# Kernel optimization log

Hardware: AMD Instinct MI355X
Metric: run time of the kernel (lower is better)

Reference implementation:

```python
import jax, jax.numpy as jnp
import numpy as np

B, N, C, NT = 32, 512, 32, 24   # batch, frames, channels-per-token, tokens
H, DH = 8, 48                   # heads, dim_head (DH % NT == 0 -> CS = 2)
E = H * DH                      # encode_dim = 384
IN = C * NT                     # in_dim = 768
OUT = 768                       # out_dim


def setup_inputs() -> dict:
    key = jax.random.key(0)
    ks = jax.random.split(key, 12)
    s = lambda fan_in: 1.0 / np.sqrt(fan_in)
    return {
        "x": jax.random.normal(ks[0], (B, N, C, NT), dtype=jnp.float32),
        "Wqkv_t": jax.random.uniform(ks[1], (IN, 3 * E), jnp.float32, -s(IN), s(IN)),
        "bqkv_t": jax.random.uniform(ks[2], (3 * E,), jnp.float32, -s(IN), s(IN)),
        "Wqkv_s": jax.random.uniform(ks[3], (IN, 3 * E), jnp.float32, -s(IN), s(IN)),
        "bqkv_s": jax.random.uniform(ks[4], (3 * E,), jnp.float32, -s(IN), s(IN)),
        "Wts": jax.random.uniform(ks[5], (2 * E, 2 * E), jnp.float32, -s(2 * E), s(2 * E)),
        "bts": jax.random.uniform(ks[6], (2 * E,), jnp.float32, -s(2 * E), s(2 * E)),
        "Wfc_t": jax.random.uniform(ks[7], (E, OUT), jnp.float32, -s(E), s(E)),
        "bfc_t": jax.random.uniform(ks[8], (OUT,), jnp.float32, -s(E), s(E)),
        "Wfc_s": jax.random.uniform(ks[9], (E, OUT), jnp.float32, -s(E), s(E)),
        "bfc_s": jax.random.uniform(ks[10], (OUT,), jnp.float32, -s(E), s(E)),
    }


def reference(x, Wqkv_t, bqkv_t, Wqkv_s, bqkv_s, Wts, bts, Wfc_t, bfc_t, Wfc_s, bfc_s):
    b, n, c, nt = x.shape
    cs = DH // nt  # channels per token inside a head (=2)
    xf = x.reshape(b, n, c * nt)                       # (b, n, in_dim)

    # --- temporal attention over the n (frame) axis ---
    qkv_t = (xf @ Wqkv_t + bqkv_t).reshape(b, n, 3, H, DH)
    qkv_t = jnp.transpose(qkv_t, (2, 0, 3, 1, 4))      # (3, b, H, n, DH)
    qt, kt, vt = qkv_t[0], qkv_t[1], qkv_t[2]
    attn_t = jax.nn.softmax(
        jnp.einsum('bhnd,bhmd->bhnm', qt, kt) / jnp.sqrt(jnp.float32(DH)), axis=-1)
    x_t = jnp.einsum('bhnm,bhmd->bnhd', attn_t, vt).reshape(b, n, E)

    # --- spatial attention over the nt (token) axis (note: unscaled, per source) ---
    qkv_s = (xf @ Wqkv_s + bqkv_s).reshape(b, n, 3, H, DH)
    qkv_s = jnp.transpose(qkv_s, (2, 0, 1, 3, 4)).reshape(3, b * n, H, cs, nt)
    qs, ks_, vs = qkv_s[0], qkv_s[1], qkv_s[2]         # (b*n, H, cs, nt)
    attn_s = jax.nn.softmax(jnp.einsum('ghct,ghcu->ghtu', qs, ks_), axis=-1)
    x_s = jnp.einsum('ghtu,ghcu->ghct', attn_s, vs)     # (b*n, H, cs, nt)
    x_s = x_s.reshape(b * n, H, cs * nt).reshape(b, n, E)

    # --- learned gating fusion ---
    alpha = jnp.concatenate([x_t, x_s], axis=-1).mean(axis=1, keepdims=True)  # (b,1,2E)
    alpha = (alpha @ Wts + bts).reshape(b, 1, E, 2)
    alpha = jax.nn.softmax(alpha, axis=-1)
    y = (x_t * alpha[:, :, :, 0]) @ Wfc_t + bfc_t + (x_s * alpha[:, :, :, 1]) @ Wfc_s + bfc_s
    return y  # dropout is identity in inference
```

## Files before the change

kernel.cpp:

```cpp
#include <hip/hip_runtime.h>
#include <hip/hip_bf16.h>


typedef __attribute__((ext_vector_type(8))) short s16x8;
typedef __attribute__((ext_vector_type(4))) float f32x4;

__device__ __forceinline__ float lo2f(uint u) { return __uint_as_float(u << 16); }
__device__ __forceinline__ float hi2f(uint u) { return __uint_as_float(u & 0xffff0000u); }
__device__ __forceinline__ ushort f2bu(float f) {
    union { __hip_bfloat16 h; ushort u; } c; c.h = __float2bfloat16(f); return c.u;
}
__device__ __forceinline__ uint pk2(float a, float b) {
    return (uint)f2bu(a) | ((uint)f2bu(b) << 16);
}
__device__ __forceinline__ void gload16(const void* g, void* l) {
    __builtin_amdgcn_global_load_lds((const __attribute__((address_space(1))) void*)g,
                                     (__attribute__((address_space(3))) void*)l, 16, 0, 0);
}

__global__ __launch_bounds__(256) void concat_bias(
    const float* __restrict__ a, const float* __restrict__ b, float* __restrict__ o)
{
    const int i = blockIdx.x * 256 + threadIdx.x;
    o[i] = (i < 1152) ? a[i] : b[i - 1152];
}

__global__ __launch_bounds__(256) void transpose_w(
    const float* __restrict__ W, ushort* __restrict__ Bt,
    int K, int N, int Kt, int koff, int noff)
{
    __shared__ float t[32][33];
    const int k0 = blockIdx.x * 32, n0 = blockIdx.y * 32;
    const int r = threadIdx.x >> 3, cq = threadIdx.x & 7;
    float4 v = *(const float4*)(W + (size_t)(k0 + r) * N + n0 + cq * 4);
    t[r][cq * 4 + 0] = v.x; t[r][cq * 4 + 1] = v.y;
    t[r][cq * 4 + 2] = v.z; t[r][cq * 4 + 3] = v.w;
    __syncthreads();
    ushort4 o;
    o.x = f2bu(t[cq * 4 + 0][r]); o.y = f2bu(t[cq * 4 + 1][r]);
    o.z = f2bu(t[cq * 4 + 2][r]); o.w = f2bu(t[cq * 4 + 3][r]);
    *(ushort4*)(Bt + (size_t)(noff + n0 + r) * Kt + koff + k0 + cq * 4) = o;
}

template<int OUTBF16, int NBIAS, int AMODE>
__global__ __launch_bounds__(512, 2) void gemm256(
    const void* __restrict__ Aw, const ushort* __restrict__ Bt,
    const float* __restrict__ bias0, const float* __restrict__ bias1,
    const float* __restrict__ gate, void* __restrict__ Cout,
    int M, int N, int K)
{
    __shared__ ushort smem[65536];
    __shared__ float gs[AMODE == 2 ? 768 : 4];
    const int tid = threadIdx.x;
    const int m0 = blockIdx.x * 256;
    const int n0 = blockIdx.y * 256;
    const int lane = tid & 63;
    const int wid = tid >> 6;
    const int wr = wid >> 2;
    const int wc = wid & 3;
    const int lr = lane & 15;
    const int g = lane >> 4;

    if (AMODE == 2) {
        const float* gsrc = gate + (size_t)(m0 >> 9) * 768;
        for (int i = tid; i < 768; i += 512) gs[i] = gsrc[i];
    }

    f32x4 acc[8][4];
#pragma unroll
    for (int i = 0; i < 8; ++i)
#pragma unroll
        for (int j = 0; j < 4; ++j) acc[i][j] = (f32x4){0.f, 0.f, 0.f, 0.f};

    int rowT[4], kqs[4];
#pragma unroll
    for (int i = 0; i < 4; ++i) {
        const int task = tid + 512 * i;
        rowT[i] = task >> 3;
        kqs[i] = (task & 7) ^ (rowT[i] & 7);
    }

    const float* Af = (const float*)Aw;
    const ushort* Ab = (const ushort*)Aw;
    float va1[4][8];
    uint4 va2[4];

    auto stageB = [&](int buf, int k0) {
        ushort* d = &smem[buf * 32768 + 16384];
#pragma unroll
        for (int i = 0; i < 4; ++i)
            gload16(Bt + (size_t)(n0 + rowT[i]) * K + k0 + (kqs[i] << 3),
                    d + (tid + 512 * i) * 8);
    };
    auto loadA = [&](int k0) {
#pragma unroll
        for (int i = 0; i < 4; ++i) {
            if (AMODE == 1) {
                const float* s = Af + (size_t)(m0 + rowT[i]) * K + k0 + (kqs[i] << 3);
                *(float4*)&va1[i][0] = *(const float4*)s;
                *(float4*)&va1[i][4] = *(const float4*)(s + 4);
            } else {
                va2[i] = *(const uint4*)(Ab + (size_t)(m0 + rowT[i]) * K + k0
                                         + (kqs[i] << 3));
            }
        }
    };
    auto writeA = [&](int buf, int k0) {
        ushort* d = &smem[buf * 32768];
#pragma unroll
        for (int i = 0; i < 4; ++i) {
            uint4 o;
            if (AMODE == 1) {
                o.x = pk2(va1[i][0], va1[i][1]);
                o.y = pk2(va1[i][2], va1[i][3]);
                o.z = pk2(va1[i][4], va1[i][5]);
                o.w = pk2(va1[i][6], va1[i][7]);
            } else {
                const float* gp = &gs[k0 + (kqs[i] << 3)];
                o.x = pk2(lo2f(va2[i].x) * gp[0], hi2f(va2[i].x) * gp[1]);
                o.y = pk2(lo2f(va2[i].y) * gp[2], hi2f(va2[i].y) * gp[3]);
                o.z = pk2(lo2f(va2[i].z) * gp[4], hi2f(va2[i].z) * gp[5]);
                o.w = pk2(lo2f(va2[i].w) * gp[6], hi2f(va2[i].w) * gp[7]);
            }
            *(uint4*)&d[(tid + 512 * i) * 8] = o;
        }
    };

    stageB(0, 0);
    loadA(0);
    __syncthreads();
    writeA(0, 0);
    __syncthreads();

    const int nt = K >> 6;
    for (int t = 0; t < nt; ++t) {
        const int cur = t & 1;
        const bool pf = (t + 1) < nt;
        if (pf) { stageB(cur ^ 1, (t + 1) << 6); loadA((t + 1) << 6); }

        const ushort* As = &smem[cur * 32768];
        const ushort* Bs = &smem[cur * 32768 + 16384];
#pragma unroll
        for (int half = 0; half < 2; ++half) {
            s16x8 bfv[4], af[8];
#pragma unroll
            for (int j = 0; j < 4; ++j) {
                const int row = wc * 64 + 16 * j + lr;
                bfv[j] = *(const s16x8*)&Bs[row * 64
                          + (((4 * half + g) ^ (row & 7)) << 3)];
            }
#pragma unroll
            for (int i = 0; i < 8; ++i) {
                const int row = wr * 128 + 16 * i + lr;
                af[i] = *(const s16x8*)&As[row * 64
                         + (((4 * half + g) ^ (row & 7)) << 3)];
            }
#pragma unroll
            for (int i = 0; i < 8; ++i)
#pragma unroll
                for (int j = 0; j < 4; ++j)
                    acc[i][j] = __builtin_amdgcn_mfma_f32_16x16x32_bf16(
                        af[i], bfv[j], acc[i][j], 0, 0, 0);
        }
        __syncthreads();
        if (pf) {
            writeA(cur ^ 1, (t + 1) << 6);
            __syncthreads();
        }
    }

    const int c0 = n0 + wc * 64 + lr;
    float bsum[4];
#pragma unroll
    for (int j = 0; j < 4; ++j) {
        bsum[j] = bias0[c0 + 16 * j];
        if (NBIAS == 2) bsum[j] += bias1[c0 + 16 * j];
    }
    const int r0 = m0 + wr * 128 + g * 4;
#pragma unroll
    for (int i = 0; i < 8; ++i) {
        const int row = r0 + 16 * i;
#pragma unroll
        for (int j = 0; j < 4; ++j) {
            const int col = c0 + 16 * j;
#pragma unroll
            for (int v = 0; v < 4; ++v) {
                const float val = acc[i][j][v] + bsum[j];
                if (OUTBF16)
                    ((ushort*)Cout)[(size_t)(row + v) * N + col] = f2bu(val);
                else
                    ((float*)Cout)[(size_t)(row + v) * N + col] = val;
            }
        }
    }
}

__global__ __launch_bounds__(256, 4) void attn_temporal(
    const ushort* __restrict__ qkv, ushort* __restrict__ xcat)
{
    const int wg = blockIdx.x;
    const int cx = wg & 7, rx = wg >> 3;
    const int id = ((rx >> 2) << 5) + 4 * cx + (rx & 3);
    const int qt = id & 3;
    const int h = (id >> 2) & 7;
    const int b = id >> 5;

    const int tid = threadIdx.x;
    const int w = tid >> 6;
    const int lane = tid & 63;
    const int lr = lane & 15;
    const int g = lane >> 4;

    __shared__ ushort Ks[64 * 64];
    __shared__ ushort Vt[48 * 64];
    __shared__ ushort Pl[4][32 * 72];
    uint* KsU = (uint*)Ks;
    uint* VtU = (uint*)Vt;

    ((uint4*)Ks)[tid] = make_uint4(0u, 0u, 0u, 0u);
    ((uint4*)Ks)[256 + tid] = make_uint4(0u, 0u, 0u, 0u);
    __syncthreads();

    const uint* qkvu = (const uint*)qkv;
    const int qrow0 = qt * 128 + w * 32;

    s16x8 qf[2][2];
#pragma unroll
    for (int n = 0; n < 2; ++n) {
        const size_t rb = (size_t)(b * 512 + qrow0 + 16 * n + lr) * 2304 + h * 48 + 8 * g;
        qf[n][0] = *(const s16x8*)(qkv + rb);
        qf[n][1] = (g < 2) ? *(const s16x8*)(qkv + rb + 32)
                           : (s16x8){0, 0, 0, 0, 0, 0, 0, 0};
    }

    int p_[3], du_[3];
#pragma unroll
    for (int i = 0; i < 3; ++i) {
        const int idx = tid + 256 * i;
        p_[i] = idx / 24;
        du_[i] = idx % 24;
    }
    uint rk[3][2], rv[3][2];

    auto stage_load = [&](int kv0) {
#pragma unroll
        for (int i = 0; i < 3; ++i) {
            const uint* s0 = qkvu + (size_t)(b * 512 + kv0 + 2 * p_[i]) * 1152
                                  + 192 + h * 24 + du_[i];
            rk[i][0] = s0[0];    rk[i][1] = s0[1152];
            rv[i][0] = s0[192];  rv[i][1] = s0[192 + 1152];
        }
    };
    auto stage_write = [&]() {
#pragma unroll
        for (int i = 0; i < 3; ++i) {
            const int p = p_[i], du = du_[i];
            KsU[(2 * p) * 32 + ((((du >> 2) ^ ((2 * p) & 7)) << 2) | (du & 3))] = rk[i][0];
            KsU[(2 * p + 1) * 32 + ((((du >> 2) ^ ((2 * p + 1) & 7)) << 2) | (du & 3))] = rk[i][1];
            const uint w0 = (rv[i][0] & 0xffffu) | (rv[i][1] << 16);
            const uint w1 = (rv[i][0] >> 16) | (rv[i][1] & 0xffff0000u);
            const int vb = (((p >> 2) ^ (du & 7)) << 2) | (p & 3);
            VtU[(2 * du) * 32 + vb] = w0;
            VtU[(2 * du + 1) * 32 + vb] = w1;
        }
    };

    f32x4 o[2][3];
#pragma unroll
    for (int mq = 0; mq < 2; ++mq)
#pragma unroll
        for (int nd = 0; nd < 3; ++nd) o[mq][nd] = (f32x4){0.f, 0.f, 0.f, 0.f};
    float mrun[2] = {-3.0e38f, -3.0e38f};
    float lsum[2] = {0.f, 0.f};
    float corrv[2];
    const float scale = 0.14433756729740643f;

    stage_load(0);
    stage_write();
    __syncthreads();

    for (int t = 0; t < 8; ++t) {
        if (t < 7) stage_load((t + 1) * 64);

        f32x4 sa[4][2];
#pragma unroll
        for (int m = 0; m < 4; ++m)
#pragma unroll
            for (int n = 0; n < 2; ++n) sa[m][n] = (f32x4){0.f, 0.f, 0.f, 0.f};
#pragma unroll
        for (int ks = 0; ks < 2; ++ks)
#pragma unroll
            for (int m = 0; m < 4; ++m) {
                s16x8 kf = *(const s16x8*)&Ks[(16 * m + lr) * 64
                                              + (((g + 4 * ks) ^ (lr & 7)) << 3)];
#pragma unroll
                for (int n = 0; n < 2; ++n)
                    sa[m][n] = __builtin_amdgcn_mfma_f32_16x16x32_bf16(
                        kf, qf[n][ks], sa[m][n], 0, 0, 0);
            }

#pragma unroll
        for (int n = 0; n < 2; ++n) {
            float tmax = -3.0e38f;
#pragma unroll
            for (int m = 0; m < 4; ++m)
#pragma unroll
                for (int v = 0; v < 4; ++v) tmax = fmaxf(tmax, sa[m][n][v]);
            tmax = fmaxf(tmax, __shfl_xor(tmax, 16));
            tmax = fmaxf(tmax, __shfl_xor(tmax, 32));
            float mnew = fmaxf(mrun[n], tmax * scale);
            float corr = __expf(mrun[n] - mnew);
            mrun[n] = mnew;
            float psum = 0.f;
#pragma unroll
            for (int m = 0; m < 4; ++m) {
                float p0 = __expf(fmaf(sa[m][n][0], scale, -mnew));
                float p1 = __expf(fmaf(sa[m][n][1], scale, -mnew));
                float p2 = __expf(fmaf(sa[m][n][2], scale, -mnew));
                float p3 = __expf(fmaf(sa[m][n][3], scale, -mnew));
                psum += (p0 + p1) + (p2 + p3);
                const int base = (16 * n + lr) * 72 + 16 * m + 4 * g;
                *(uint*)&Pl[w][base] = pk2(p0, p1);
                *(uint*)&Pl[w][base + 2] = pk2(p2, p3);
            }
            psum += __shfl_xor(psum, 16);
            psum += __shfl_xor(psum, 32);
            lsum[n] = lsum[n] * corr + psum;
            corrv[n] = corr;
        }

#pragma unroll
        for (int mq = 0; mq < 2; ++mq)
#pragma unroll
            for (int nd = 0; nd < 3; ++nd)
#pragma unroll
                for (int v = 0; v < 4; ++v) o[mq][nd][v] *= corrv[mq];

#pragma unroll
        for (int ks = 0; ks < 2; ++ks) {
            s16x8 vf[3];
#pragma unroll
            for (int nd = 0; nd < 3; ++nd)
                vf[nd] = *(const s16x8*)&Vt[(16 * nd + lr) * 64
                                            + (((g + 4 * ks) ^ (lr >> 1)) << 3)];
#pragma unroll
            for (int mq = 0; mq < 2; ++mq) {
                s16x8 pf = *(const s16x8*)&Pl[w][(16 * mq + lr) * 72 + 8 * g + 32 * ks];
#pragma unroll
                for (int nd = 0; nd < 3; ++nd)
                    o[mq][nd] = __builtin_amdgcn_mfma_f32_16x16x32_bf16(
                        vf[nd], pf, o[mq][nd], 0, 0, 0);
            }
        }
        __syncthreads();
        if (t < 7) stage_write();
        __syncthreads();
    }

#pragma unroll
    for (int mq = 0; mq < 2; ++mq) {
        const float li = 1.f / lsum[mq];
        const int qrow = qrow0 + 16 * mq + lr;
        ushort* dst = xcat + (size_t)(b * 512 + qrow) * 768 + h * 48;
#pragma unroll
        for (int nd = 0; nd < 3; ++nd) {
            uint2 o2;
            o2.x = pk2(o[mq][nd][0] * li, o[mq][nd][1] * li);
            o2.y = pk2(o[mq][nd][2] * li, o[mq][nd][3] * li);
            *(uint2*)(dst + 16 * nd + 4 * g) = o2;
        }
    }
}

__global__ __launch_bounds__(192) void attn_spatial(
    const ushort* __restrict__ qkv, ushort* __restrict__ xcat)
{
    const int g = blockIdx.x;
    __shared__ float row[1152];
    const uint* qkvu = (const uint*)qkv;
#pragma unroll
    for (int i = 0; i < 3; ++i) {
        int idx = threadIdx.x + 192 * i;
        uint u = qkvu[(size_t)g * 1152 + 576 + idx];
        row[2 * idx] = lo2f(u); row[2 * idx + 1] = hi2f(u);
    }
    __syncthreads();

    const int h = threadIdx.x / 24;
    const int t = threadIdx.x % 24;
    const float* q = &row[h * 48];
    const float* k = &row[384 + h * 48];
    const float* v = &row[768 + h * 48];
    const float q0 = q[t], q1 = q[24 + t];

    float s[24];
    float mx = -3.0e38f;
#pragma unroll
    for (int u = 0; u < 24; ++u) {
        s[u] = q0 * k[u] + q1 * k[24 + u];
        mx = fmaxf(mx, s[u]);
    }
    float l = 0.f;
#pragma unroll
    for (int u = 0; u < 24; ++u) { s[u] = __expf(s[u] - mx); l += s[u]; }
    const float inv = 1.f / l;
    float o0 = 0.f, o1 = 0.f;
#pragma unroll
    for (int u = 0; u < 24; ++u) {
        o0 = fmaf(s[u], v[u], o0);
        o1 = fmaf(s[u], v[24 + u], o1);
    }
    ushort* dst = xcat + (size_t)g * 768 + 384 + h * 48;
    dst[t] = f2bu(o0 * inv);
    dst[24 + t] = f2bu(o1 * inv);
}

__global__ __launch_bounds__(256) void colsum(
    const ushort* __restrict__ xcat, float* __restrict__ partial)
{
    const int b = blockIdx.x, ch = blockIdx.y, part = blockIdx.z;
    const int e = ch * 256 + threadIdx.x;
    const int n0 = part * 64;
    float s = 0.f;
    for (int n = 0; n < 64; ++n)
        s += __uint_as_float((uint)xcat[((size_t)(b * 512 + n0 + n)) * 768 + e] << 16);
    partial[((size_t)(b * 8 + part)) * 768 + e] = s;
}

__global__ __launch_bounds__(256) void alpha_gate(
    const float* __restrict__ partial, const float* __restrict__ Wts,
    const float* __restrict__ bts, float* __restrict__ gate)
{
    const int b = blockIdx.x;
    const int j0 = blockIdx.y * 128;
    __shared__ float av[768];
    __shared__ float psum[2][128];

    for (int i = threadIdx.x; i < 768; i += 256) {
        float s = 0.f;
#pragma unroll
        for (int p = 0; p < 8; ++p)
            s += partial[((size_t)(b * 8 + p)) * 768 + i];
        av[i] = s * (1.0f / 512.0f);
    }
    __syncthreads();

    const int jl = threadIdx.x & 127;
    const int seg = threadIdx.x >> 7;
    const int j = j0 + jl;
    const float* Wp = Wts + (size_t)(seg * 384) * 768 + j;
    const float* avp = av + seg * 384;
    float a0 = 0.f, a1 = 0.f, a2 = 0.f, a3 = 0.f;
    float a4 = 0.f, a5 = 0.f, a6 = 0.f, a7 = 0.f;
#pragma unroll 4
    for (int k = 0; k < 384; k += 8) {
        a0 = fmaf(avp[k + 0], Wp[(size_t)(k + 0) * 768], a0);
        a1 = fmaf(avp[k + 1], Wp[(size_t)(k + 1) * 768], a1);
        a2 = fmaf(avp[k + 2], Wp[(size_t)(k + 2) * 768], a2);
        a3 = fmaf(avp[k + 3], Wp[(size_t)(k + 3) * 768], a3);
        a4 = fmaf(avp[k + 4], Wp[(size_t)(k + 4) * 768], a4);
        a5 = fmaf(avp[k + 5], Wp[(size_t)(k + 5) * 768], a5);
        a6 = fmaf(avp[k + 6], Wp[(size_t)(k + 6) * 768], a6);
        a7 = fmaf(avp[k + 7], Wp[(size_t)(k + 7) * 768], a7);
    }
    psum[seg][jl] = ((a0 + a1) + (a2 + a3)) + ((a4 + a5) + (a6 + a7));
    __syncthreads();

    if (threadIdx.x < 128)
        av[threadIdx.x] = psum[0][threadIdx.x] + psum[1][threadIdx.x]
                        + bts[j0 + threadIdx.x];
    __syncthreads();
    if (threadIdx.x < 64) {
        const int e = (j0 >> 1) + threadIdx.x;
        float x0 = av[2 * threadIdx.x], x1 = av[2 * threadIdx.x + 1];
        float m = fmaxf(x0, x1);
        float e0 = __expf(x0 - m), e1 = __expf(x1 - m);
        float inv = 1.f / (e0 + e1);
        gate[(size_t)b * 768 + e] = e0 * inv;
        gate[(size_t)b * 768 + 384 + e] = e1 * inv;
    }
}

extern "C" void kernel_launch(void* const* d_in, const int* in_sizes, int n_in,
                              void* d_out, int out_size, void* d_ws, size_t ws_size,
                              hipStream_t stream)
{
    const float* x      = (const float*)d_in[0];
    const float* Wqkv_t = (const float*)d_in[1];
    const float* bqkv_t = (const float*)d_in[2];
    const float* Wqkv_s = (const float*)d_in[3];
    const float* bqkv_s = (const float*)d_in[4];
    const float* Wts    = (const float*)d_in[5];
    const float* bts    = (const float*)d_in[6];
    const float* Wfc_t  = (const float*)d_in[7];
    const float* bfc_t  = (const float*)d_in[8];
    const float* Wfc_s  = (const float*)d_in[9];
    const float* bfc_s  = (const float*)d_in[10];
    float* out = (float*)d_out;

    char* w = (char*)d_ws;
    ushort* qkv2   = (ushort*)(w);
    ushort* xcat   = (ushort*)(w + 75497472);
    ushort* wbuf   = (ushort*)(w + 100663296);
    ushort* wbuf2  = (ushort*)(w + 104202240);
    float*  partial= (float*)(w + 105381888);
    float*  gate   = (float*)(w + 106168320);
    float*  bias2  = (float*)(w + 106266624);

    const dim3 blk256(256);

    concat_bias<<<dim3(9), blk256, 0, stream>>>(bqkv_t, bqkv_s, bias2);
    transpose_w<<<dim3(24, 36), blk256, 0, stream>>>(Wqkv_t, wbuf, 768, 1152, 768, 0, 0);
    transpose_w<<<dim3(24, 36), blk256, 0, stream>>>(Wqkv_s, wbuf, 768, 1152, 768, 0, 1152);

    gemm256<1, 1, 1><<<dim3(64, 9), dim3(512), 0, stream>>>(
        x, wbuf, bias2, nullptr, nullptr, qkv2, 16384, 2304, 768);

    attn_temporal<<<dim3(1024), blk256, 0, stream>>>(qkv2, xcat);
    attn_spatial<<<dim3(16384), dim3(192), 0, stream>>>(qkv2, xcat);

    colsum<<<dim3(32, 3, 8), blk256, 0, stream>>>(xcat, partial);
    alpha_gate<<<dim3(32, 6), blk256, 0, stream>>>(partial, Wts, bts, gate);

    transpose_w<<<dim3(12, 24), blk256, 0, stream>>>(Wfc_t, wbuf2, 384, 768, 768, 0, 0);
    transpose_w<<<dim3(12, 24), blk256, 0, stream>>>(Wfc_s, wbuf2, 384, 768, 768, 384, 0);
    gemm256<0, 2, 2><<<dim3(64, 3), dim3(512), 0, stream>>>(
        xcat, wbuf2, bfc_t, bfc_s, gate, out, 16384, 768, 768);
}
```

Before: 237.4 us.

## Pre-convert GEMM operands to bf16 and use 128x128 async-staged GEMM

Adds separate passes that convert x to bf16 and apply the gate to xcat ahead of time. Both GEMMs can then load A and B directly into LDS via global_load_lds, with double buffering and vmcnt-based waits in place of register staging. The GEMM tile shrinks from 256x256 with 512 threads to 128x128 with 256 threads, giving more blocks and better CU occupancy. The cost is two extra elementwise kernels that add global memory traffic, since x is read and written again and the gated copy of xcat is materialised.

```diff
diff --git a/kernel.cpp b/kernel.cpp
--- a/kernel.cpp
+++ b/kernel.cpp
@@ -16,6 +16,18 @@
 __device__ __forceinline__ void gload16(const void* g, void* l) {
     __builtin_amdgcn_global_load_lds((const __attribute__((address_space(1))) void*)g,
                                      (__attribute__((address_space(3))) void*)l, 16, 0, 0);
+}
+
+__global__ __launch_bounds__(256) void convert_bf16(
+    const float* __restrict__ in, ushort* __restrict__ out)
+{
+    const int i = blockIdx.x * 256 + threadIdx.x;
+    const float4* p = (const float4*)in + (size_t)i * 2;
+    float4 a = p[0], b = p[1];
+    uint4 o;
+    o.x = pk2(a.x, a.y); o.y = pk2(a.z, a.w);
+    o.z = pk2(b.x, b.y); o.w = pk2(b.z, b.w);
+    ((uint4*)out)[i] = o;
 }
 
 __global__ __launch_bounds__(256) void concat_bias(
@@ -42,107 +54,73 @@
     *(ushort4*)(Bt + (size_t)(noff + n0 + r) * Kt + koff + k0 + cq * 4) = o;
 }
 
-template<int OUTBF16, int NBIAS, int AMODE>
-__global__ __launch_bounds__(512, 2) void gemm256(
-    const void* __restrict__ Aw, const ushort* __restrict__ Bt,
+template<int OUTBF16, int NBIAS>
+__global__ __launch_bounds__(256, 2) void gemm128p(
+    const ushort* __restrict__ A, const ushort* __restrict__ Bt,
     const float* __restrict__ bias0, const float* __restrict__ bias1,
-    const float* __restrict__ gate, void* __restrict__ Cout,
-    int M, int N, int K)
-{
-    __shared__ ushort smem[65536];
-    __shared__ float gs[AMODE == 2 ? 768 : 4];
+    void* __restrict__ Cout, int M, int N, int K)
+{
+    __shared__ ushort smem[32768];
     const int tid = threadIdx.x;
-    const int m0 = blockIdx.x * 256;
-    const int n0 = blockIdx.y * 256;
+    const int m0 = blockIdx.x * 128;
+    const int n0 = blockIdx.y * 128;
     const int lane = tid & 63;
-    const int wid = tid >> 6;
-    const int wr = wid >> 2;
-    const int wc = wid & 3;
+    const int wr = tid >> 7;
+    const int wc = (tid >> 6) & 1;
     const int lr = lane & 15;
     const int g = lane >> 4;
 
-    if (AMODE == 2) {
-        const float* gsrc = gate + (size_t)(m0 >> 9) * 768;
-        for (int i = tid; i < 768; i += 512) gs[i] = gsrc[i];
-    }
-
-    f32x4 acc[8][4];
-#pragma unroll
-    for (int i = 0; i < 8; ++i)
+    f32x4 acc[4][4];
+#pragma unroll
+    for (int i = 0; i < 4; ++i)
 #pragma unroll
         for (int j = 0; j < 4; ++j) acc[i][j] = (f32x4){0.f, 0.f, 0.f, 0.f};
 
     int rowT[4], kqs[4];
 #pragma unroll
     for (int i = 0; i < 4; ++i) {
-        const int task = tid + 512 * i;
+        const int task = tid + 256 * i;
         rowT[i] = task >> 3;
         kqs[i] = (task & 7) ^ (rowT[i] & 7);
     }
 
-    const float* Af = (const float*)Aw;
-    const ushort* Ab = (const ushort*)Aw;
-    float va1[4][8];
-    uint4 va2[4];
-
-    auto stageB = [&](int buf, int k0) {
-        ushort* d = &smem[buf * 32768 + 16384];
-#pragma unroll
-        for (int i = 0; i < 4; ++i)
+    auto stage = [&](int buf, int k0) {
+        ushort* dA = &smem[buf * 16384];
+        ushort* dB = &smem[buf * 16384 + 8192];
+#pragma unroll
+        for (int i = 0; i < 4; ++i) {
+            gload16(A + (size_t)(m0 + rowT[i]) * K + k0 + (kqs[i] << 3),
+                    dA + (tid + 256 * i) * 8);
             gload16(Bt + (size_t)(n0 + rowT[i]) * K + k0 + (kqs[i] << 3),
-                    d + (tid + 512 * i) * 8);
+                    dB + (tid + 256 * i) * 8);
+        }
     };
-    auto loadA = [&](int k0) {
-#pragma unroll
-        for (int i = 0; i < 4; ++i) {
-            if (AMODE == 1) {
-                const float* s = Af + (size_t)(m0 + rowT[i]) * K + k0 + (kqs[i] << 3);
-                *(float4*)&va1[i][0] = *(const float4*)s;
-                *(float4*)&va1[i][4] = *(const float4*)(s + 4);
-            } else {
-                va2[i] = *(const uint4*)(Ab + (size_t)(m0 + rowT[i]) * K + k0
-                                         + (kqs[i] << 3));
-            }
-        }
-    };
-    auto writeA = [&](int buf, int k0) {
-        ushort* d = &smem[buf * 32768];
-#pragma unroll
-        for (int i = 0; i < 4; ++i) {
-            uint4 o;
-            if (AMODE == 1) {
-                o.x = pk2(va1[i][0], va1[i][1]);
-                o.y = pk2(va1[i][2], va1[i][3]);
-                o.z = pk2(va1[i][4], va1[i][5]);
-                o.w = pk2(va1[i][6], va1[i][7]);
-            } else {
-                const float* gp = &gs[k0 + (kqs[i] << 3)];
-                o.x = pk2(lo2f(va2[i].x) * gp[0], hi2f(va2[i].x) * gp[1]);
-                o.y = pk2(lo2f(va2[i].y) * gp[2], hi2f(va2[i].y) * gp[3]);
-                o.z = pk2(lo2f(va2[i].z) * gp[4], hi2f(va2[i].z) * gp[5]);
-                o.w = pk2(lo2f(va2[i].w) * gp[6], hi2f(va2[i].w) * gp[7]);
-            }
-            *(uint4*)&d[(tid + 512 * i) * 8] = o;
-        }
-    };
-
-    stageB(0, 0);
-    loadA(0);
-    __syncthreads();
-    writeA(0, 0);
-    __syncthreads();
-
+
+    stage(0, 0);
     const int nt = K >> 6;
     for (int t = 0; t < nt; ++t) {
         const int cur = t & 1;
-        const bool pf = (t + 1) < nt;
-        if (pf) { stageB(cur ^ 1, (t + 1) << 6); loadA((t + 1) << 6); }
-
-        const ushort* As = &smem[cur * 32768];
-        const ushort* Bs = &smem[cur * 32768 + 16384];
+        if (t + 1 < nt) {
+            stage(cur ^ 1, (t + 1) << 6);
+            asm volatile("s_waitcnt vmcnt(8)" ::: "memory");
+        } else {
+            asm volatile("s_waitcnt vmcnt(0)" ::: "memory");
+        }
+        __builtin_amdgcn_sched_barrier(0);
+        __builtin_amdgcn_s_barrier();
+        __builtin_amdgcn_sched_barrier(0);
+
+        const ushort* As = &smem[cur * 16384];
+        const ushort* Bs = &smem[cur * 16384 + 8192];
 #pragma unroll
         for (int half = 0; half < 2; ++half) {
-            s16x8 bfv[4], af[8];
+            s16x8 af[4], bfv[4];
+#pragma unroll
+            for (int i = 0; i < 4; ++i) {
+                const int row = wr * 64 + 16 * i + lr;
+                af[i] = *(const s16x8*)&As[row * 64
+                         + (((4 * half + g) ^ (row & 7)) << 3)];
+            }
 #pragma unroll
             for (int j = 0; j < 4; ++j) {
                 const int row = wc * 64 + 16 * j + lr;
@@ -150,23 +128,14 @@
                           + (((4 * half + g) ^ (row & 7)) << 3)];
             }
 #pragma unroll
-            for (int i = 0; i < 8; ++i) {
-                const int row = wr * 128 + 16 * i + lr;
-                af[i] = *(const s16x8*)&As[row * 64
-                         + (((4 * half + g) ^ (row & 7)) << 3)];
-            }
-#pragma unroll
-            for (int i = 0; i < 8; ++i)
+            for (int i = 0; i < 4; ++i)
 #pragma unroll
                 for (int j = 0; j < 4; ++j)
                     acc[i][j] = __builtin_amdgcn_mfma_f32_16x16x32_bf16(
                         af[i], bfv[j], acc[i][j], 0, 0, 0);
         }
-        __syncthreads();
-        if (pf) {
-            writeA(cur ^ 1, (t + 1) << 6);
-            __syncthreads();
-        }
+        __builtin_amdgcn_sched_barrier(0);
+        __builtin_amdgcn_s_barrier();
     }
 
     const int c0 = n0 + wc * 64 + lr;
@@ -176,9 +145,9 @@
         bsum[j] = bias0[c0 + 16 * j];
         if (NBIAS == 2) bsum[j] += bias1[c0 + 16 * j];
     }
-    const int r0 = m0 + wr * 128 + g * 4;
-#pragma unroll
-    for (int i = 0; i < 8; ++i) {
+    const int r0 = m0 + wr * 64 + g * 4;
+#pragma unroll
+    for (int i = 0; i < 4; ++i) {
         const int row = r0 + 16 * i;
 #pragma unroll
         for (int j = 0; j < 4; ++j) {
@@ -481,6 +450,26 @@
     }
 }
 
+__global__ __launch_bounds__(256) void gate_mul(
+    const ushort* __restrict__ xcat, const float* __restrict__ gate,
+    ushort* __restrict__ xg)
+{
+    const int i = blockIdx.x * 256 + threadIdx.x;
+    const int m = i / 96;
+    const int k = (i % 96) * 8;
+    const int b = m >> 9;
+    uint4 u = ((const uint4*)xcat)[i];
+    const float* g = gate + (size_t)b * 768 + k;
+    float4 g0 = *(const float4*)g;
+    float4 g1 = *(const float4*)(g + 4);
+    uint4 o;
+    o.x = pk2(lo2f(u.x) * g0.x, hi2f(u.x) * g0.y);
+    o.y = pk2(lo2f(u.y) * g0.z, hi2f(u.y) * g0.w);
+    o.z = pk2(lo2f(u.z) * g1.x, hi2f(u.z) * g1.y);
+    o.w = pk2(lo2f(u.w) * g1.z, hi2f(u.w) * g1.w);
+    ((uint4*)xg)[i] = o;
+}
+
 extern "C" void kernel_launch(void* const* d_in, const int* in_sizes, int n_in,
                               void* d_out, int out_size, void* d_ws, size_t ws_size,
                               hipStream_t stream)
@@ -500,30 +489,34 @@
 
     char* w = (char*)d_ws;
     ushort* qkv2   = (ushort*)(w);
+    ushort* xg     = qkv2;
     ushort* xcat   = (ushort*)(w + 75497472);
-    ushort* wbuf   = (ushort*)(w + 100663296);
-    ushort* wbuf2  = (ushort*)(w + 104202240);
-    float*  partial= (float*)(w + 105381888);
-    float*  gate   = (float*)(w + 106168320);
-    float*  bias2  = (float*)(w + 106266624);
+    ushort* xb     = (ushort*)(w + 100663296);
+    ushort* wbuf   = (ushort*)(w + 125829120);
+    ushort* wbuf2  = (ushort*)(w + 129368064);
+    float*  partial= (float*)(w + 130547712);
+    float*  gate   = (float*)(w + 131334144);
+    float*  bias2  = (float*)(w + 131432448);
 
     const dim3 blk256(256);
 
+    convert_bf16<<<dim3(6144), blk256, 0, stream>>>(x, xb);
     concat_bias<<<dim3(9), blk256, 0, stream>>>(bqkv_t, bqkv_s, bias2);
     transpose_w<<<dim3(24, 36), blk256, 0, stream>>>(Wqkv_t, wbuf, 768, 1152, 768, 0, 0);
     transpose_w<<<dim3(24, 36), blk256, 0, stream>>>(Wqkv_s, wbuf, 768, 1152, 768, 0, 1152);
 
-    gemm256<1, 1, 1><<<dim3(64, 9), dim3(512), 0, stream>>>(
-        x, wbuf, bias2, nullptr, nullptr, qkv2, 16384, 2304, 768);
+    gemm128p<1, 1><<<dim3(128, 18), blk256, 0, stream>>>(
+        xb, wbuf, bias2, nullptr, qkv2, 16384, 2304, 768);
 
     attn_temporal<<<dim3(1024), blk256, 0, stream>>>(qkv2, xcat);
     attn_spatial<<<dim3(16384), dim3(192), 0, stream>>>(qkv2, xcat);
 
     colsum<<<dim3(32, 3, 8), blk256, 0, stream>>>(xcat, partial);
     alpha_gate<<<dim3(32, 6), blk256, 0, stream>>>(partial, Wts, bts, gate);
+    gate_mul<<<dim3(6144), blk256, 0, stream>>>(xcat, gate, xg);
 
     transpose_w<<<dim3(12, 24), blk256, 0, stream>>>(Wfc_t, wbuf2, 384, 768, 768, 0, 0);
     transpose_w<<<dim3(12, 24), blk256, 0, stream>>>(Wfc_s, wbuf2, 384, 768, 768, 384, 0);
-    gemm256<0, 2, 2><<<dim3(64, 3), dim3(512), 0, stream>>>(
-        xcat, wbuf2, bfc_t, bfc_s, gate, out, 16384, 768, 768);
-}
+    gemm128p<0, 2><<<dim3(128, 6), blk256, 0, stream>>>(
+        xg, wbuf2, bfc_t, bfc_s, out, 16384, 768, 768);
+}
```

After: 200.5 us. -15.5%, faster.
